# Performance work log

Hardware: AMD Instinct MI355X
Metric: run time of the kernel (lower is better)

Reference implementation:

```python
import jax, jax.numpy as jnp
import numpy as np

HEAD_DIM = 512 // (8 * 2)  # in_dim // (num_heads * 2) = 32
SQRT2 = np.sqrt(2.0).astype(np.float32)


def dwt1d_haar(x):
    # Haar DWT along last dim: L=(even+odd)/sqrt2, H=(even-odd)/sqrt2
    xe, xo = x[..., 0::2], x[..., 1::2]
    return (xe + xo) / SQRT2, (xe - xo) / SQRT2


def idwt1d_haar(L, H):
    # Inverse: even=(L+H)/sqrt2, odd=(L-H)/sqrt2, interleaved
    even = (L + H) / SQRT2
    odd = (L - H) / SQRT2
    x = jnp.stack([even, odd], axis=-1)  # [..., D/2, 2]
    return x.reshape(*x.shape[:-2], -1)  # [..., D]


def setup_inputs() -> dict:
    key = jax.random.key(0)
    k1, k2, k3, k4 = jax.random.split(key, 4)
    B, S, D = 8, 2048, 512
    queries = jax.random.normal(k1, (B, S, D), dtype=jnp.float32)
    keys = jax.random.normal(k2, (B, S, D), dtype=jnp.float32)
    values = jax.random.normal(k3, (B, S, D), dtype=jnp.float32)
    W_o = jax.random.normal(k4, (D, D), dtype=jnp.float32) * (1.0 / np.sqrt(D))
    b_o = jnp.zeros((D,), dtype=jnp.float32)
    return {"queries": queries, "keys": keys, "values": values, "W_o": W_o, "b_o": b_o}


def reference(queries, keys, values, W_o, b_o):
    scale = 1.0 / jnp.sqrt(jnp.asarray(HEAD_DIM, dtype=queries.dtype))
    q_L, q_H = dwt1d_haar(queries)
    k_L, k_H = dwt1d_haar(keys)
    v_L, v_H = dwt1d_haar(values)
    # [B,S,S] score matrices for each wavelet branch
    attn_L = jax.nn.softmax(jnp.einsum("bqd,bkd->bqk", q_L, k_L) * scale, axis=-1)
    attn_H = jax.nn.softmax(jnp.einsum("bqd,bkd->bqk", q_H, k_H) * scale, axis=-1)
    L_out = jnp.einsum("bqk,bkd->bqd", attn_L, v_L)
    H_out = jnp.einsum("bqk,bkd->bqd", attn_H, v_H)
    output = idwt1d_haar(L_out, H_out)  # [B,S,D]
    return output @ W_o.T + b_o
```

## Files before the change

kernel.cpp:

```cpp
#include <hip/hip_runtime.h>

#define INV_SQRT2 0.70710678118654752f
#define QSCALE    0.17677669529663689f
#define LOG2E     1.44269504088896340f
#define SM_SHIFT  32.0f

typedef __attribute__((ext_vector_type(8))) short bf16x8;
typedef __attribute__((ext_vector_type(4))) float f32x4;
typedef __attribute__((ext_vector_type(16))) float f32x16;

__device__ __forceinline__ unsigned pack2bf(float a, float b) {
  union { float f; unsigned u; } ua, ub; ua.f = a; ub.f = b;
  unsigned ra = ua.u + 0x7FFFu + ((ua.u >> 16) & 1u);
  unsigned rb = ub.u + 0x7FFFu + ((ub.u >> 16) & 1u);
  return __builtin_amdgcn_perm(rb, ra, 0x07060302);
}

__device__ __forceinline__ float exp2_raw(float x) {
  float r;
  asm("v_exp_f32 %0, %1" : "=v"(r) : "v"(x));
  return r;
}

__device__ __forceinline__ void async16(const short* g, short* l) {
  typedef __attribute__((address_space(3))) unsigned lds_u32;
  typedef const __attribute__((address_space(1))) unsigned glb_u32;
  __builtin_amdgcn_global_load_lds((glb_u32*)g, (lds_u32*)l, 16, 0, 0);
}

__global__ void dwt_all(const float* __restrict__ q, const float* __restrict__ k,
                        const float* __restrict__ v, const float* __restrict__ W,
                        short* __restrict__ qs, short* __restrict__ ks,
                        short* __restrict__ vt, short* __restrict__ w2) {
  __shared__ float tL[64][65];
  __shared__ float tH[64][65];
  int bi = blockIdx.x;
  int t = threadIdx.x;
  if (bi < 2048) {
    int idx = bi * 256 + t;
    int j = idx & 31;
    int s = (idx >> 5) & 2047;
    int b = idx >> 16;
    const float4* qp = (const float4*)(q + ((size_t)(b * 2048 + s)) * 512 + j * 16);
    const float4* kp = (const float4*)(k + ((size_t)(b * 2048 + s)) * 512 + j * 16);
    float4 a0 = qp[0], a1 = qp[1], a2 = qp[2], a3 = qp[3];
    float4 c0 = kp[0], c1 = kp[1], c2 = kp[2], c3 = kp[3];
    union { bf16x8 v; unsigned u[4]; } qL, qH, kL, kH;
    const float cs = INV_SQRT2 * QSCALE * LOG2E;
    qL.u[0] = pack2bf((a0.x + a0.y) * cs, (a0.z + a0.w) * cs);
    qL.u[1] = pack2bf((a1.x + a1.y) * cs, (a1.z + a1.w) * cs);
    qL.u[2] = pack2bf((a2.x + a2.y) * cs, (a2.z + a2.w) * cs);
    qL.u[3] = pack2bf((a3.x + a3.y) * cs, (a3.z + a3.w) * cs);
    qH.u[0] = pack2bf((a0.x - a0.y) * cs, (a0.z - a0.w) * cs);
    qH.u[1] = pack2bf((a1.x - a1.y) * cs, (a1.z - a1.w) * cs);
    qH.u[2] = pack2bf((a2.x - a2.y) * cs, (a2.z - a2.w) * cs);
    qH.u[3] = pack2bf((a3.x - a3.y) * cs, (a3.z - a3.w) * cs);
    kL.u[0] = pack2bf((c0.x + c0.y) * INV_SQRT2, (c0.z + c0.w) * INV_SQRT2);
    kL.u[1] = pack2bf((c1.x + c1.y) * INV_SQRT2, (c1.z + c1.w) * INV_SQRT2);
    kL.u[2] = pack2bf((c2.x + c2.y) * INV_SQRT2, (c2.z + c2.w) * INV_SQRT2);
    kL.u[3] = pack2bf((c3.x + c3.y) * INV_SQRT2, (c3.z + c3.w) * INV_SQRT2);
    kH.u[0] = pack2bf((c0.x - c0.y) * INV_SQRT2, (c0.z - c0.w) * INV_SQRT2);
    kH.u[1] = pack2bf((c1.x - c1.y) * INV_SQRT2, (c1.z - c1.w) * INV_SQRT2);
    kH.u[2] = pack2bf((c2.x - c2.y) * INV_SQRT2, (c2.z - c2.w) * INV_SQRT2);
    kH.u[3] = pack2bf((c3.x - c3.y) * INV_SQRT2, (c3.z - c3.w) * INV_SQRT2);
    size_t oL = ((size_t)(b * 2) * 2048 + s) * 256 + j * 8;
    size_t oH = oL + (size_t)2048 * 256;
    *(bf16x8*)(qs + oL) = qL.v;  *(bf16x8*)(qs + oH) = qH.v;
    *(bf16x8*)(ks + oL) = kL.v;  *(bf16x8*)(ks + oH) = kH.v;
  } else if (bi < 3072) {
    int bi2 = bi - 2048;
    int it = bi2 & 3, st = (bi2 >> 2) & 31, b = bi2 >> 7;
#pragma unroll
    for (int rep = 0; rep < 8; rep++) {
      int unit = rep * 256 + t;
      int r = unit >> 5, cp = (unit & 31) * 2;
      float4 vv = *(const float4*)(v + ((size_t)(b * 2048 + st * 64 + r)) * 512 + it * 128 + cp * 2);
      tL[r][cp]     = (vv.x + vv.y) * INV_SQRT2;
      tL[r][cp + 1] = (vv.z + vv.w) * INV_SQRT2;
      tH[r][cp]     = (vv.x - vv.y) * INV_SQRT2;
      tH[r][cp + 1] = (vv.z - vv.w) * INV_SQRT2;
    }
    __syncthreads();
#pragma unroll
    for (int rep = 0; rep < 2; rep++) {
      int unit = rep * 256 + t;
      int i = unit >> 3, cc = unit & 7;
      union { bf16x8 v; unsigned u[4]; } pL, pH;
#pragma unroll
      for (int p = 0; p < 4; p++) {
        pL.u[p] = pack2bf(tL[cc * 8 + p * 2][i], tL[cc * 8 + p * 2 + 1][i]);
        pH.u[p] = pack2bf(tH[cc * 8 + p * 2][i], tH[cc * 8 + p * 2 + 1][i]);
      }
      size_t o = ((size_t)(b * 2) * 256 + it * 64 + i) * 2048 + st * 64 + cc * 8;
      *(bf16x8*)(vt + o) = pL.v;
      *(bf16x8*)(vt + o + (size_t)256 * 2048) = pH.v;
    }
  } else {
    int idx = (bi - 3072) * 256 + t;
    int j = idx >> 6, i4 = (idx & 63) * 4;
    const float4* src = (const float4*)(W + (size_t)j * 512 + 2 * i4);
    float4 f0 = src[0], f1 = src[1];
    uint2 dl, dh;
    dl.x = pack2bf((f0.x + f0.y) * INV_SQRT2, (f0.z + f0.w) * INV_SQRT2);
    dl.y = pack2bf((f1.x + f1.y) * INV_SQRT2, (f1.z + f1.w) * INV_SQRT2);
    dh.x = pack2bf((f0.x - f0.y) * INV_SQRT2, (f0.z - f0.w) * INV_SQRT2);
    dh.y = pack2bf((f1.x - f1.y) * INV_SQRT2, (f1.z - f1.w) * INV_SQRT2);
    *(uint2*)(w2 + (size_t)j * 512 + i4) = dl;
    *(uint2*)(w2 + (size_t)j * 512 + 256 + i4) = dh;
  }
}

__launch_bounds__(256, 2)
__global__ void flash_attn(const short* __restrict__ qs, const short* __restrict__ ks,
                           const short* __restrict__ vt, short* __restrict__ os) {
  __shared__ short lds[36864];
  short* klds = lds;
  short* vlds = lds + 16384;
  short* plds = lds + 32768;

  int tid = threadIdx.x;
  int w = tid >> 6, L = tid & 63;
  int lq = L & 31, hi = L >> 5;
  int qt = w & 1, ct = w >> 1;
  int bb = blockIdx.x, qb = blockIdx.y;

  bf16x8 qf[16];
  const short* qptr = qs + (((size_t)bb * 2048) + qb * 64 + qt * 32 + lq) * 256 + hi * 8;
#pragma unroll
  for (int ksI = 0; ksI < 16; ksI++)
    qf[ksI] = *(const bf16x8*)(qptr + ksI * 16);

  f32x16 oacc[4];
#pragma unroll
  for (int mt = 0; mt < 4; mt++)
#pragma unroll
    for (int i = 0; i < 16; i++) oacc[mt][i] = 0.f;
  float l_i = 0.f;

  const short* kbase = ks + ((size_t)bb * 2048) * 256;
  const short* vbase = vt + ((size_t)bb * 256) * 2048;

  int krow = ct * 32 + lq, ksw = krow & 7;
  int qrow = qt * 32 + lq, qsw = qrow & 7;
  int sw8 = lq & 7;

  const short* kaddr[16];
#pragma unroll
  for (int i = 0; i < 16; i++)
    kaddr[i] = klds + krow * 256 + (((i << 1) | hi) ^ ksw) * 8;
  short* pwr[4];
#pragma unroll
  for (int g = 0; g < 4; g++)
    pwr[g] = plds + qrow * 64 + ((4 * ct + g) ^ qsw) * 8 + hi * 4;
  const short* prd[4];
#pragma unroll
  for (int i = 0; i < 4; i++)
    prd[i] = plds + qrow * 64 + (((i << 1) | hi) ^ qsw) * 8;
  int vch[4];
#pragma unroll
  for (int i = 0; i < 4; i++)
    vch[i] = (((i << 1) | hi) ^ sw8) * 8;
  const short* vrowp[4];
#pragma unroll
  for (int mt = 0; mt < 4; mt++)
    vrowp[mt] = vlds + (ct * 128 + mt * 32 + lq) * 64;

  const short* kp[8];
  const short* vp[8];
#pragma unroll
  for (int rep = 0; rep < 8; rep++) {
    int o = w * 8 + rep;
    int r = 2 * o + (L >> 5);
    int c = (L & 31) ^ (r & 7);
    kp[rep] = kbase + r * 256 + c * 8;
    int n = 8 * o + (L >> 3);
    int cv = (L & 7) ^ (n & 7);
    vp[rep] = vbase + n * 2048 + cv * 8;
  }

#pragma unroll
  for (int rep = 0; rep < 8; rep++) {
    async16(kp[rep], klds + (w * 8 + rep) * 512);
    kp[rep] += 16384;
  }
  __syncthreads();

  for (int kt = 0; kt < 32; kt++) {
#pragma unroll
    for (int rep = 0; rep < 8; rep++) {
      async16(vp[rep], vlds + (w * 8 + rep) * 512);
      vp[rep] += 64;
    }

    f32x16 s0, s1;
#pragma unroll
    for (int i = 0; i < 16; i++) { s0[i] = 0.f; s1[i] = 0.f; }
#pragma unroll
    for (int ksI = 0; ksI < 16; ksI += 2) {
      bf16x8 kb0 = *(const bf16x8*)kaddr[ksI];
      bf16x8 kb1 = *(const bf16x8*)kaddr[ksI + 1];
      s0 = __builtin_amdgcn_mfma_f32_32x32x16_bf16(kb0, qf[ksI], s0, 0, 0, 0);
      s1 = __builtin_amdgcn_mfma_f32_32x32x16_bf16(kb1, qf[ksI + 1], s1, 0, 0, 0);
    }

    float rs = 0.f;
#pragma unroll
    for (int g = 0; g < 4; g++) {
      float p0 = exp2_raw(s0[4 * g]     + s1[4 * g]     - SM_SHIFT);
      float p1 = exp2_raw(s0[4 * g + 1] + s1[4 * g + 1] - SM_SHIFT);
      float p2 = exp2_raw(s0[4 * g + 2] + s1[4 * g + 2] - SM_SHIFT);
      float p3 = exp2_raw(s0[4 * g + 3] + s1[4 * g + 3] - SM_SHIFT);
      rs += (p0 + p1) + (p2 + p3);
      uint2 d; d.x = pack2bf(p0, p1); d.y = pack2bf(p2, p3);
      *(uint2*)pwr[g] = d;
    }
    l_i += rs;
    __syncthreads();

    if (kt < 31) {
#pragma unroll
      for (int rep = 0; rep < 8; rep++) {
        async16(kp[rep], klds + (w * 8 + rep) * 512);
        kp[rep] += 16384;
      }
    }

    bf16x8 pb[4];
#pragma unroll
    for (int ks4 = 0; ks4 < 4; ks4++)
      pb[ks4] = *(const bf16x8*)prd[ks4];
#pragma unroll
    for (int mt = 0; mt < 4; mt++) {
#pragma unroll
      for (int ks4 = 0; ks4 < 4; ks4++) {
        bf16x8 vb = *(const bf16x8*)(vrowp[mt] + vch[ks4]);
        oacc[mt] = __builtin_amdgcn_mfma_f32_32x32x16_bf16(vb, pb[ks4], oacc[mt], 0, 0, 0);
      }
    }
    __syncthreads();
  }

  float lt = l_i + __shfl_xor(l_i, 32, 64);
  float* lbuf = (float*)plds;
  if (hi == 0) lbuf[(ct * 2 + qt) * 32 + lq] = lt;
  __syncthreads();
  float inv = 1.f / (lt + lbuf[((ct ^ 1) * 2 + qt) * 32 + lq]);

#pragma unroll
  for (int mt = 0; mt < 4; mt++)
#pragma unroll
    for (int g = 0; g < 4; g++) {
      uint2 d;
      d.x = pack2bf(oacc[mt][4 * g] * inv, oacc[mt][4 * g + 1] * inv);
      d.y = pack2bf(oacc[mt][4 * g + 2] * inv, oacc[mt][4 * g + 3] * inv);
      *(uint2*)(lds + qrow * 264 + ct * 128 + mt * 32 + 8 * g + 4 * hi) = d;
    }
  __syncthreads();
  short* obase = os + (((size_t)bb * 2048) + qb * 64) * 256;
#pragma unroll
  for (int rep = 0; rep < 8; rep++) {
    int cid = rep * 256 + tid;
    int row = cid >> 5, c = cid & 31;
    *(bf16x8*)(obase + row * 256 + c * 8) = *(const bf16x8*)(lds + row * 264 + c * 8);
  }
}

__launch_bounds__(256, 2)
__global__ void out_gemm(const short* __restrict__ os, const short* __restrict__ w2,
                         const float* __restrict__ bo, float* __restrict__ out) {
  __shared__ short alds[128 * 72];
  __shared__ short blds[128 * 72];
  int tid = threadIdx.x;
  int w = tid >> 6, L = tid & 63, lo = L & 15, hi = L >> 4;
  int wr = w >> 1, wc = w & 1;
  int br = blockIdx.x, bc = blockIdx.y;

  f32x4 acc[4][4];
#pragma unroll
  for (int mt = 0; mt < 4; mt++)
#pragma unroll
    for (int nt = 0; nt < 4; nt++)
      acc[mt][nt] = (f32x4){0.f, 0.f, 0.f, 0.f};

  for (int kt = 0; kt < 8; kt++) {
    __syncthreads();
#pragma unroll
    for (int rep = 0; rep < 4; rep++) {
      int cid = rep * 256 + tid;
      int mrow = cid >> 3, c = cid & 7;
      int gk = kt * 64 + c * 8;
      int half = gk >> 8, i = gk & 255;
      int gr = br * 128 + mrow;
      int b = gr >> 11, s = gr & 2047;
      *(bf16x8*)(alds + mrow * 72 + c * 8) =
          *(const bf16x8*)(os + ((size_t)((b * 2 + half) * 2048 + s)) * 256 + i);
    }
#pragma unroll
    for (int rep = 0; rep < 4; rep++) {
      int cid = rep * 256 + tid;
      int nrow = cid >> 3, c = cid & 7;
      *(bf16x8*)(blds + nrow * 72 + c * 8) =
          *(const bf16x8*)(w2 + (size_t)(bc * 128 + nrow) * 512 + kt * 64 + c * 8);
    }
    __syncthreads();
    bf16x8 af[4], bfr[4];
#pragma unroll
    for (int kc = 0; kc < 2; kc++) {
#pragma unroll
      for (int mt = 0; mt < 4; mt++)
        af[mt] = *(const bf16x8*)(alds + (wr * 64 + mt * 16 + lo) * 72 + kc * 32 + hi * 8);
#pragma unroll
      for (int nt = 0; nt < 4; nt++)
        bfr[nt] = *(const bf16x8*)(blds + (wc * 64 + nt * 16 + lo) * 72 + kc * 32 + hi * 8);
#pragma unroll
      for (int mt = 0; mt < 4; mt++)
#pragma unroll
        for (int nt = 0; nt < 4; nt++)
          acc[mt][nt] = __builtin_amdgcn_mfma_f32_16x16x32_bf16(af[mt], bfr[nt], acc[mt][nt], 0, 0, 0);
    }
  }

#pragma unroll
  for (int nt = 0; nt < 4; nt++) {
    int cc = bc * 128 + wc * 64 + nt * 16 + lo;
    float bias = bo[cc];
#pragma unroll
    for (int mt = 0; mt < 4; mt++) {
      int rrbase = br * 128 + wr * 64 + mt * 16 + hi * 4;
#pragma unroll
      for (int r = 0; r < 4; r++)
        out[(size_t)(rrbase + r) * 512 + cc] = acc[mt][nt][r] + bias;
    }
  }
}

extern "C" void kernel_launch(void* const* d_in, const int* in_sizes, int n_in,
                              void* d_out, int out_size, void* d_ws, size_t ws_size,
                              hipStream_t stream) {
  const float* q  = (const float*)d_in[0];
  const float* k  = (const float*)d_in[1];
  const float* v  = (const float*)d_in[2];
  const float* W  = (const float*)d_in[3];
  const float* bo = (const float*)d_in[4];
  short* ws  = (short*)d_ws;
  short* qs  = ws;
  short* ksb = ws + (size_t)8  * 1024 * 1024;
  short* vtp = ws + (size_t)16 * 1024 * 1024;
  short* osb = ws + (size_t)24 * 1024 * 1024;
  short* w2  = ws + (size_t)32 * 1024 * 1024;

  dwt_all<<<3200, 256, 0, stream>>>(q, k, v, W, qs, ksb, vtp, w2);
  flash_attn<<<dim3(16, 32), 256, 0, stream>>>(qs, ksb, vtp, osb);
  out_gemm<<<dim3(128, 4), 256, 0, stream>>>(osb, w2, bo, (float*)d_out);
}
```

Before: 248.6 us.

## Remap PV MFMA tiling per wave and double-buffer out_gemm with async loads

```diff
diff --git a/kernel.cpp b/kernel.cpp
--- a/kernel.cpp
+++ b/kernel.cpp
@@ -152,18 +152,22 @@
 #pragma unroll
   for (int g = 0; g < 4; g++)
     pwr[g] = plds + qrow * 64 + ((4 * ct + g) ^ qsw) * 8 + hi * 4;
-  const short* prd[4];
-#pragma unroll
-  for (int i = 0; i < 4; i++)
-    prd[i] = plds + qrow * 64 + (((i << 1) | hi) ^ qsw) * 8;
+  const short* prdA[4];
+  const short* prdB[4];
+#pragma unroll
+  for (int i = 0; i < 4; i++) {
+    int ch = (((i << 1) | hi) ^ sw8) * 8;
+    prdA[i] = plds + lq * 64 + ch;
+    prdB[i] = plds + (32 + lq) * 64 + ch;
+  }
   int vch[4];
 #pragma unroll
   for (int i = 0; i < 4; i++)
     vch[i] = (((i << 1) | hi) ^ sw8) * 8;
-  const short* vrowp[4];
-#pragma unroll
-  for (int mt = 0; mt < 4; mt++)
-    vrowp[mt] = vlds + (ct * 128 + mt * 32 + lq) * 64;
+  const short* vrowp[2];
+#pragma unroll
+  for (int dt = 0; dt < 2; dt++)
+    vrowp[dt] = vlds + (w * 64 + dt * 32 + lq) * 64;
 
   const short* kp[8];
   const short* vp[8];
@@ -225,16 +229,19 @@
       }
     }
 
-    bf16x8 pb[4];
-#pragma unroll
-    for (int ks4 = 0; ks4 < 4; ks4++)
-      pb[ks4] = *(const bf16x8*)prd[ks4];
-#pragma unroll
-    for (int mt = 0; mt < 4; mt++) {
-#pragma unroll
-      for (int ks4 = 0; ks4 < 4; ks4++) {
-        bf16x8 vb = *(const bf16x8*)(vrowp[mt] + vch[ks4]);
-        oacc[mt] = __builtin_amdgcn_mfma_f32_32x32x16_bf16(vb, pb[ks4], oacc[mt], 0, 0, 0);
+    bf16x8 pa[4], pb[4];
+#pragma unroll
+    for (int i = 0; i < 4; i++) {
+      pa[i] = *(const bf16x8*)prdA[i];
+      pb[i] = *(const bf16x8*)prdB[i];
+    }
+#pragma unroll
+    for (int dt = 0; dt < 2; dt++) {
+#pragma unroll
+      for (int i = 0; i < 4; i++) {
+        bf16x8 vb = *(const bf16x8*)(vrowp[dt] + vch[i]);
+        oacc[dt * 2]     = __builtin_amdgcn_mfma_f32_32x32x16_bf16(vb, pa[i], oacc[dt * 2], 0, 0, 0);
+        oacc[dt * 2 + 1] = __builtin_amdgcn_mfma_f32_32x32x16_bf16(vb, pb[i], oacc[dt * 2 + 1], 0, 0, 0);
       }
     }
     __syncthreads();
@@ -244,17 +251,22 @@
   float* lbuf = (float*)plds;
   if (hi == 0) lbuf[(ct * 2 + qt) * 32 + lq] = lt;
   __syncthreads();
-  float inv = 1.f / (lt + lbuf[((ct ^ 1) * 2 + qt) * 32 + lq]);
-
-#pragma unroll
-  for (int mt = 0; mt < 4; mt++)
+  float inv0 = 1.f / (lbuf[lq] + lbuf[64 + lq]);
+  float inv1 = 1.f / (lbuf[32 + lq] + lbuf[96 + lq]);
+
+#pragma unroll
+  for (int ot = 0; ot < 4; ot++) {
+    int qt2 = ot & 1, dt = ot >> 1;
+    float inv = qt2 ? inv1 : inv0;
+    int qg = qt2 * 32 + lq;
 #pragma unroll
     for (int g = 0; g < 4; g++) {
       uint2 d;
-      d.x = pack2bf(oacc[mt][4 * g] * inv, oacc[mt][4 * g + 1] * inv);
-      d.y = pack2bf(oacc[mt][4 * g + 2] * inv, oacc[mt][4 * g + 3] * inv);
-      *(uint2*)(lds + qrow * 264 + ct * 128 + mt * 32 + 8 * g + 4 * hi) = d;
-    }
+      d.x = pack2bf(oacc[ot][4 * g] * inv, oacc[ot][4 * g + 1] * inv);
+      d.y = pack2bf(oacc[ot][4 * g + 2] * inv, oacc[ot][4 * g + 3] * inv);
+      *(uint2*)(lds + qg * 264 + w * 64 + dt * 32 + 8 * g + 4 * hi) = d;
+    }
+  }
   __syncthreads();
   short* obase = os + (((size_t)bb * 2048) + qb * 64) * 256;
 #pragma unroll
@@ -268,13 +280,26 @@
 __launch_bounds__(256, 2)
 __global__ void out_gemm(const short* __restrict__ os, const short* __restrict__ w2,
                          const float* __restrict__ bo, float* __restrict__ out) {
-  __shared__ short alds[128 * 72];
-  __shared__ short blds[128 * 72];
+  __shared__ short alds[2][8192];
+  __shared__ short blds[2][8192];
   int tid = threadIdx.x;
   int w = tid >> 6, L = tid & 63, lo = L & 15, hi = L >> 4;
   int wr = w >> 1, wc = w & 1;
   int br = blockIdx.x, bc = blockIdx.y;
 
+  int rrow[4], rchk[4];
+#pragma unroll
+  for (int rep = 0; rep < 4; rep++) {
+    int o = w * 4 + rep;
+    int r = o * 8 + (L >> 3);
+    rrow[rep] = r;
+    rchk[rep] = ((L & 7) ^ (r & 7)) * 8;
+  }
+  int b = br >> 4;
+  int s0 = (br & 15) * 128;
+  const short* abase = os + ((size_t)(b * 2) * 2048 + s0) * 256;
+  const short* bbase = w2 + (size_t)(bc * 128) * 512;
+
   f32x4 acc[4][4];
 #pragma unroll
   for (int mt = 0; mt < 4; mt++)
@@ -282,42 +307,47 @@
     for (int nt = 0; nt < 4; nt++)
       acc[mt][nt] = (f32x4){0.f, 0.f, 0.f, 0.f};
 
+  int fch[2];
+#pragma unroll
+  for (int kc = 0; kc < 2; kc++)
+    fch[kc] = ((kc * 4 + hi) ^ (lo & 7)) * 8;
+
+#pragma unroll
+  for (int rep = 0; rep < 4; rep++) {
+    async16(abase + rrow[rep] * 256 + rchk[rep], &alds[0][(w * 4 + rep) * 512] + L * 8);
+    async16(bbase + rrow[rep] * 512 + rchk[rep], &blds[0][(w * 4 + rep) * 512] + L * 8);
+  }
+  __syncthreads();
+
+  int p = 0;
   for (int kt = 0; kt < 8; kt++) {
-    __syncthreads();
-#pragma unroll
-    for (int rep = 0; rep < 4; rep++) {
-      int cid = rep * 256 + tid;
-      int mrow = cid >> 3, c = cid & 7;
-      int gk = kt * 64 + c * 8;
-      int half = gk >> 8, i = gk & 255;
-      int gr = br * 128 + mrow;
-      int b = gr >> 11, s = gr & 2047;
-      *(bf16x8*)(alds + mrow * 72 + c * 8) =
-          *(const bf16x8*)(os + ((size_t)((b * 2 + half) * 2048 + s)) * 256 + i);
-    }
-#pragma unroll
-    for (int rep = 0; rep < 4; rep++) {
-      int cid = rep * 256 + tid;
-      int nrow = cid >> 3, c = cid & 7;
-      *(bf16x8*)(blds + nrow * 72 + c * 8) =
-          *(const bf16x8*)(w2 + (size_t)(bc * 128 + nrow) * 512 + kt * 64 + c * 8);
-    }
-    __syncthreads();
+    if (kt < 7) {
+      int k1 = kt + 1;
+      int half = k1 >> 2, i0 = (k1 & 3) * 64;
+      const short* ab = abase + (size_t)half * 2048 * 256 + i0;
+#pragma unroll
+      for (int rep = 0; rep < 4; rep++) {
+        async16(ab + rrow[rep] * 256 + rchk[rep], &alds[p ^ 1][(w * 4 + rep) * 512] + L * 8);
+        async16(bbase + rrow[rep] * 512 + k1 * 64 + rchk[rep], &blds[p ^ 1][(w * 4 + rep) * 512] + L * 8);
+      }
+    }
     bf16x8 af[4], bfr[4];
 #pragma unroll
     for (int kc = 0; kc < 2; kc++) {
 #pragma unroll
       for (int mt = 0; mt < 4; mt++)
-        af[mt] = *(const bf16x8*)(alds + (wr * 64 + mt * 16 + lo) * 72 + kc * 32 + hi * 8);
+        af[mt] = *(const bf16x8*)(&alds[p][(wr * 64 + mt * 16 + lo) * 64 + fch[kc]]);
 #pragma unroll
       for (int nt = 0; nt < 4; nt++)
-        bfr[nt] = *(const bf16x8*)(blds + (wc * 64 + nt * 16 + lo) * 72 + kc * 32 + hi * 8);
+        bfr[nt] = *(const bf16x8*)(&blds[p][(wc * 64 + nt * 16 + lo) * 64 + fch[kc]]);
 #pragma unroll
       for (int mt = 0; mt < 4; mt++)
 #pragma unroll
         for (int nt = 0; nt < 4; nt++)
           acc[mt][nt] = __builtin_amdgcn_mfma_f32_16x16x32_bf16(af[mt], bfr[nt], acc[mt][nt], 0, 0, 0);
     }
+    __syncthreads();
+    p ^= 1;
   }
 
 #pragma unroll
```

Result: faster. 242.3 us (-2.5%).
